# Optimization experiments

Hardware: AMD Instinct MI355X
Metric: run time of the kernel (lower is better)

## Reference

```python
import jax, jax.numpy as jnp
import numpy as np

TEMPERATURE = 1.0
EPS = 1e-8


def setup_inputs() -> dict:
    key = jax.random.key(0)
    k1, k2, k3 = jax.random.split(key, 3)
    B, N = 32768, 32
    scores = jax.random.normal(k1, (B, N), dtype=jnp.float32)
    rankings = jax.random.randint(k2, (B, N), 0, 32, dtype=jnp.int64)
    mask = jax.random.randint(k3, (B, N), 0, 2) > 0
    return {"scores": scores, "rankings": rankings, "mask": mask}


def reference(scores, rankings, mask):
    # scores: [B, N] float, rankings: [B, N] int (0 => unranked), mask: [B, N] bool
    s = scores / TEMPERATURE
    valid = mask & (rankings > 0)                      # [B, N]

    ri = rankings[:, :, None]                          # [B, N, 1]
    rj = rankings[:, None, :]                          # [B, 1, N]
    # i==j implies ri==rj, so (ri != rj) also excludes the diagonal
    pair_valid = (valid[:, :, None] & valid[:, None, :] & (ri != rj))  # [B, N, N]

    p_ij = (ri < rj).astype(s.dtype)                   # target probability
    s_ij = jax.nn.sigmoid(s[:, :, None] - s[:, None, :])
    pair_loss = -p_ij * jnp.log(s_ij + EPS) - (1.0 - p_ij) * jnp.log(1.0 - s_ij + EPS)

    pv = pair_valid.astype(s.dtype)
    per_batch_sum = jnp.sum(pair_loss * pv, axis=(1, 2))     # [B]
    num_pairs = jnp.sum(pv, axis=(1, 2))                     # [B]

    has_pairs = num_pairs > 0
    per_batch_loss = jnp.where(has_pairs, per_batch_sum / jnp.maximum(num_pairs, 1.0), 0.0)
    n_batches = jnp.sum(has_pairs.astype(s.dtype))
    # reduction='mean' over batches that contributed pairs; 0.0 if none
    return jnp.where(n_batches > 0, jnp.sum(per_batch_loss) / jnp.maximum(n_batches, 1.0), 0.0)
```

## Files before the change

kernel.cpp:

```cpp
#include <hip/hip_runtime.h>

__global__ __launch_bounds__(256) void ranknet_partial_kernel(
    const float* __restrict__ scores,
    const int*   __restrict__ rankings,
    const int*   __restrict__ mask,
    float2*      __restrict__ partials)
{
    const int lane = threadIdx.x & 63;
    const int wave = threadIdx.x >> 6;
    const int item = lane & 31;
    const int half = lane & 32;
    const int base = blockIdx.x * 1024;

    float pb_acc  = 0.0f;
    float has_acc = 0.0f;

    #pragma unroll
    for (int set = 0; set < 4; ++set) {
        const int idx = base + set * 256 + threadIdx.x;
        const float s = scores[idx];
        const int   r = rankings[idx];
        const int   m = mask[idx];
        const int   rr = (m != 0 && r > 0) ? r : 0;

        const unsigned su = (__float_as_uint(s) & ~31u) | (unsigned)rr;
        const float sj = __uint_as_float(su);
        const int   rj = rr;

        unsigned pk[16];
        #pragma unroll
        for (int t = 1; t <= 16; ++t)
            pk[t - 1] = __shfl(su, half | ((item + t) & 31));

        float ysum = 0.0f;
        float prod = 1.0f;
        float cnt  = 0.0f;
        #pragma unroll
        for (int t = 1; t <= 16; ++t) {
            const unsigned pu = pk[t - 1];
            const int   ri = (int)(pu & 31u);
            const float si = __uint_as_float(pu);

            const float x = si - sj;
            const float y = (ri < rj) ? -x : x;
            const float e = __expf(-fabsf(y));

            bool valid = (ri != 0) & (rj != 0) & (ri != rj);
            if (t == 16) valid = valid && (item < 16);
            ysum += valid ? fmaxf(y, 0.0f) : 0.0f;
            prod *= valid ? (1.0f + e) : 1.0f;
            cnt  += valid ? 1.0f : 0.0f;
        }
        float lsum = ysum + __logf(prod);
        float lcnt = cnt;

        #pragma unroll
        for (int off = 16; off > 0; off >>= 1) {
            lsum += __shfl_xor(lsum, off);
            lcnt += __shfl_xor(lcnt, off);
        }
        pb_acc  += (lcnt > 0.0f) ? (lsum / lcnt) : 0.0f;
        has_acc += (lcnt > 0.0f) ? 1.0f : 0.0f;
    }

    pb_acc  += __shfl_xor(pb_acc, 32);
    has_acc += __shfl_xor(has_acc, 32);

    __shared__ float2 wpart[4];
    if (lane == 0) wpart[wave] = make_float2(pb_acc, has_acc);
    __syncthreads();
    if (threadIdx.x == 0) {
        float ps = 0.0f, pc = 0.0f;
        #pragma unroll
        for (int w2 = 0; w2 < 4; ++w2) { ps += wpart[w2].x; pc += wpart[w2].y; }
        partials[blockIdx.x] = make_float2(ps, pc);
    }
}

__global__ __launch_bounds__(256) void ranknet_finalize_kernel(
    const float2* __restrict__ partials, int n, float* __restrict__ out)
{
    float s = 0.0f, c = 0.0f;
    for (int i = threadIdx.x; i < n; i += 256) {
        const float2 p = partials[i];
        s += p.x;
        c += p.y;
    }
    #pragma unroll
    for (int off = 32; off > 0; off >>= 1) {
        s += __shfl_xor(s, off);
        c += __shfl_xor(c, off);
    }
    __shared__ float2 wsum[4];
    const int wave = threadIdx.x >> 6;
    const int lane = threadIdx.x & 63;
    if (lane == 0) wsum[wave] = make_float2(s, c);
    __syncthreads();
    if (threadIdx.x == 0) {
        float ts = 0.0f, tc = 0.0f;
        #pragma unroll
        for (int w = 0; w < 4; ++w) { ts += wsum[w].x; tc += wsum[w].y; }
        out[0] = (tc > 0.0f) ? (ts / tc) : 0.0f;
    }
}

extern "C" void kernel_launch(void* const* d_in, const int* in_sizes, int n_in,
                              void* d_out, int out_size, void* d_ws, size_t ws_size,
                              hipStream_t stream) {
    const float* scores   = (const float*)d_in[0];
    const int*   rankings = (const int*)d_in[1];
    const int*   mask     = (const int*)d_in[2];
    float*       out      = (float*)d_out;

    const int total   = in_sizes[0];
    const int nblocks = total / 1024;

    float2* partials = (float2*)d_ws;

    ranknet_partial_kernel<<<nblocks, 256, 0, stream>>>(scores, rankings, mask, partials);
    ranknet_finalize_kernel<<<1, 256, 0, stream>>>(partials, nblocks, out);
}
```

Baseline: 17.23 us.

## Vectorize loads with float4 and spread each row across eight lanes

Each thread now loads four consecutive elements with 16-byte vector loads, so one 32-item row spans eight lanes instead of thirty-two. Pairwise terms are formed by shuffling packed score/rank words within the 8-lane group, and the reductions shrink accordingly. Scores are prescaled by log2(e) so exp2/log2 replace exp/log, with the scale undone at the end. This cuts load instructions and shuffle volume per pair, at the cost of more registers per thread and fewer threads sharing each row.

```diff
diff --git a/kernel.cpp b/kernel.cpp
--- a/kernel.cpp
+++ b/kernel.cpp
@@ -1,73 +1,83 @@
 #include <hip/hip_runtime.h>
 
 __global__ __launch_bounds__(256) void ranknet_partial_kernel(
-    const float* __restrict__ scores,
-    const int*   __restrict__ rankings,
-    const int*   __restrict__ mask,
-    float2*      __restrict__ partials)
+    const float4* __restrict__ scores4,
+    const int4*   __restrict__ rank4,
+    const int4*   __restrict__ mask4,
+    float2*       __restrict__ partials)
 {
+    const int gid  = blockIdx.x * 256 + threadIdx.x;
     const int lane = threadIdx.x & 63;
     const int wave = threadIdx.x >> 6;
-    const int item = lane & 31;
-    const int half = lane & 32;
-    const int base = blockIdx.x * 1024;
 
-    float pb_acc  = 0.0f;
-    float has_acc = 0.0f;
+    const float4 s4 = scores4[gid];
+    const int4   r4 = rank4[gid];
+    const int4   m4 = mask4[gid];
+
+    const float L2E = 1.4426950408889634f;
+
+    unsigned su[4];
+    int      rj[4];
+    float    rjnz[4];
+    {
+        const float sv[4] = {s4.x, s4.y, s4.z, s4.w};
+        const int   rv[4] = {r4.x, r4.y, r4.z, r4.w};
+        const int   mv[4] = {m4.x, m4.y, m4.z, m4.w};
+        #pragma unroll
+        for (int c = 0; c < 4; ++c) {
+            const int rr = (mv[c] != 0 && rv[c] > 0) ? rv[c] : 0;
+            su[c]   = (__float_as_uint(sv[c] * L2E) & ~31u) | (unsigned)rr;
+            rj[c]   = rr;
+            rjnz[c] = (rr != 0) ? 1.0f : 0.0f;
+        }
+    }
+
+    float A = 0.0f;
+    float P = 1.0f;
+    float C = 0.0f;
+
+    const bool low = ((lane & 7) < 4);
 
     #pragma unroll
-    for (int set = 0; set < 4; ++set) {
-        const int idx = base + set * 256 + threadIdx.x;
-        const float s = scores[idx];
-        const int   r = rankings[idx];
-        const int   m = mask[idx];
-        const int   rr = (m != 0 && r > 0) ? r : 0;
+    for (int t = 1; t <= 16; ++t) {
+        #pragma unroll
+        for (int c = 0; c < 4; ++c) {
+            const int delta = (t + c) >> 2;
+            const int gamma = (t + c) & 3;
+            const int src   = (lane & ~7) | ((lane + delta) & 7);
+            const unsigned pu = __shfl(su[gamma], src);
 
-        const unsigned su = (__float_as_uint(s) & ~31u) | (unsigned)rr;
-        const float sj = __uint_as_float(su);
-        const int   rj = rr;
+            const int   ri = (int)(pu & 31u);
+            const float x  = __uint_as_float(pu) - __uint_as_float(su[c]);
+            const float y  = (ri < rj[c]) ? -x : x;
+            const float e  = __builtin_exp2f(-__builtin_fabsf(x));
 
-        unsigned pk[16];
-        #pragma unroll
-        for (int t = 1; t <= 16; ++t)
-            pk[t - 1] = __shfl(su, half | ((item + t) & 31));
+            float validf = ((ri != 0) && (ri != rj[c])) ? rjnz[c] : 0.0f;
+            if (t == 16) validf = low ? validf : 0.0f;
 
-        float ysum = 0.0f;
-        float prod = 1.0f;
-        float cnt  = 0.0f;
-        #pragma unroll
-        for (int t = 1; t <= 16; ++t) {
-            const unsigned pu = pk[t - 1];
-            const int   ri = (int)(pu & 31u);
-            const float si = __uint_as_float(pu);
-
-            const float x = si - sj;
-            const float y = (ri < rj) ? -x : x;
-            const float e = __expf(-fabsf(y));
-
-            bool valid = (ri != 0) & (rj != 0) & (ri != rj);
-            if (t == 16) valid = valid && (item < 16);
-            ysum += valid ? fmaxf(y, 0.0f) : 0.0f;
-            prod *= valid ? (1.0f + e) : 1.0f;
-            cnt  += valid ? 1.0f : 0.0f;
+            A  = fmaf(validf, fmaxf(y, 0.0f), A);
+            P *= fmaf(validf, e, 1.0f);
+            C += validf;
         }
-        float lsum = ysum + __logf(prod);
-        float lcnt = cnt;
-
-        #pragma unroll
-        for (int off = 16; off > 0; off >>= 1) {
-            lsum += __shfl_xor(lsum, off);
-            lcnt += __shfl_xor(lcnt, off);
-        }
-        pb_acc  += (lcnt > 0.0f) ? (lsum / lcnt) : 0.0f;
-        has_acc += (lcnt > 0.0f) ? 1.0f : 0.0f;
     }
 
-    pb_acc  += __shfl_xor(pb_acc, 32);
-    has_acc += __shfl_xor(has_acc, 32);
+    float v = A + __builtin_log2f(P);
+    #pragma unroll
+    for (int off = 1; off <= 4; off <<= 1) {
+        v += __shfl_xor(v, off);
+        C += __shfl_xor(C, off);
+    }
+    float pb  = (C > 0.0f) ? (v * 0.6931471805599453f) / C : 0.0f;
+    float has = (C > 0.0f) ? 1.0f : 0.0f;
+
+    #pragma unroll
+    for (int off = 8; off <= 32; off <<= 1) {
+        pb  += __shfl_xor(pb, off);
+        has += __shfl_xor(has, off);
+    }
 
     __shared__ float2 wpart[4];
-    if (lane == 0) wpart[wave] = make_float2(pb_acc, has_acc);
+    if (lane == 0) wpart[wave] = make_float2(pb, has);
     __syncthreads();
     if (threadIdx.x == 0) {
         float ps = 0.0f, pc = 0.0f;
@@ -107,16 +117,16 @@
 extern "C" void kernel_launch(void* const* d_in, const int* in_sizes, int n_in,
                               void* d_out, int out_size, void* d_ws, size_t ws_size,
                               hipStream_t stream) {
-    const float* scores   = (const float*)d_in[0];
-    const int*   rankings = (const int*)d_in[1];
-    const int*   mask     = (const int*)d_in[2];
-    float*       out      = (float*)d_out;
+    const float4* scores4 = (const float4*)d_in[0];
+    const int4*   rank4   = (const int4*)d_in[1];
+    const int4*   mask4   = (const int4*)d_in[2];
+    float*        out     = (float*)d_out;
 
     const int total   = in_sizes[0];
     const int nblocks = total / 1024;
 
     float2* partials = (float2*)d_ws;
 
-    ranknet_partial_kernel<<<nblocks, 256, 0, stream>>>(scores, rankings, mask, partials);
+    ranknet_partial_kernel<<<nblocks, 256, 0, stream>>>(scores4, rank4, mask4, partials);
     ranknet_finalize_kernel<<<1, 256, 0, stream>>>(partials, nblocks, out);
 }
```

New measurement: 15.86 us. -7.9%, faster.
